# Optimization experiments

Measured on AMD Instinct MI355X. Metric: run time of the kernel, lower is better.

## Reference

```python
import jax, jax.numpy as jnp
import numpy as np

TEMP = 0.1
EPS = 1e-12  # F.normalize eps


def setup_inputs() -> dict:
    key = jax.random.key(0)
    k1, k2 = jax.random.split(key)
    B, C, N = 8, 128, 4096
    features = jax.random.normal(k1, (B, C, N), dtype=jnp.float32)
    labels_all = jax.random.randint(k2, (B, N), 0, 16, dtype=jnp.int32)
    return {"features": features, "labels_all": labels_all}


def _per_cloud_loss(features_map, labels):
    # features_map: [C, N], labels: [N]
    v = features_map.T  # [N, C]
    v = v / jnp.maximum(jnp.linalg.norm(v, axis=1, keepdims=True), EPS)
    dp = jnp.exp(jnp.matmul(v, v.T) / TEMP)  # [N, N]
    n = dp.shape[0]
    # remove diagonal (dot_products - diag(diagonal))
    dp = dp * (1.0 - jnp.eye(n, dtype=dp.dtype))
    mask = labels[:, None] == labels[None, :]  # [N, N]
    positives = jnp.sum(jnp.where(mask, dp, 0.0), axis=1)
    negatives = jnp.sum(jnp.where(mask, 0.0, dp), axis=1)
    deviation = -jnp.log(positives / (positives + negatives))
    return jnp.mean(deviation)


def reference(features, labels_all):
    # features: [B, C, N], labels_all: [B, N]
    losses = jax.vmap(_per_cloud_loss)(features, labels_all)  # [B]
    return jnp.mean(losses)
```

## Files before the change

kernel.cpp:

```cpp
#include <hip/hip_runtime.h>
#include <hip/hip_bf16.h>
#include <math.h>

#define BATCH 8
#define NPTS 4096
#define CH 128
#define CTG 4
#define CHUNK 32
#define NCHUNK (NPTS / (CTG * CHUNK))
#define NBUF 4

#define SQRT_TEMP_LOG2E 3.79828256f

typedef __attribute__((ext_vector_type(4))) float f32x4;
typedef __attribute__((ext_vector_type(4))) int   i32x4;
typedef __attribute__((ext_vector_type(8))) short bf16x8;

typedef __attribute__((address_space(3))) unsigned int lds_uint;
typedef __attribute__((address_space(1))) const unsigned int gbl_uint;

__device__ __forceinline__ void load_lds16(const void* g, const void* l) {
    __builtin_amdgcn_global_load_lds((gbl_uint*)g, (lds_uint*)l, 16, 0, 0);
}

__device__ __forceinline__ float fast_exp2(float x) {
    return __builtin_amdgcn_exp2f(x);
}

__global__ __launch_bounds__(256) void normalize_kernel(
    const float* __restrict__ f, __hip_bfloat16* __restrict__ vn,
    float* __restrict__ pos, float* __restrict__ neg, float* __restrict__ out)
{
    int idx = blockIdx.x * 256 + threadIdx.x;
    int point = idx >> 2, q = idx & 3;
    int b = point >> 12, n = point & (NPTS - 1);
    const float* base = f + (size_t)b * CH * NPTS + (size_t)(q * 32) * NPTS + n;

    float x[32];
    float ss = 0.0f;
    #pragma unroll
    for (int c = 0; c < 32; c++) {
        x[c] = base[(size_t)c * NPTS];
        ss += x[c] * x[c];
    }
    ss += __shfl_xor(ss, 1);
    ss += __shfl_xor(ss, 2);
    float scale = SQRT_TEMP_LOG2E / fmaxf(sqrtf(ss), 1e-12f);

    __hip_bfloat16* outp = vn + (size_t)point * CH + q * 32;
    #pragma unroll
    for (int c0 = 0; c0 < 32; c0 += 8) {
        union { __hip_bfloat16 h[8]; uint4 u; } pk;
        #pragma unroll
        for (int j = 0; j < 8; j++)
            pk.h[j] = __float2bfloat16(x[c0 + j] * scale);
        *((uint4*)(outp + c0)) = pk.u;
    }
    if (q == 0) pos[point] = 0.0f;
    else if (q == 1) neg[point] = 0.0f;
    if (idx == 0) out[0] = 0.0f;
}

__global__ __launch_bounds__(256, 4) void tile_kernel(
    const __hip_bfloat16* __restrict__ vn, const int* __restrict__ labels,
    float* __restrict__ pos, float* __restrict__ neg)
{
    __shared__ short lB[NBUF][CHUNK * CH];
    __shared__ int labL[NPTS / CTG];

    const int ctg = blockIdx.x, rt = blockIdx.y, b = blockIdx.z;
    const int tid = threadIdx.x;
    const int w = tid >> 6, lane = tid & 63;
    const int lane15 = lane & 15, quad = lane >> 4;

    const int row0 = rt * 128;
    const int colbase = ctg * (NPTS / CTG);
    const __hip_bfloat16* vb = vn + (size_t)b * NPTS * CH;
    const int* labb = labels + b * NPTS;

    auto STAGE = [&](int buf, int chunk) {
        const __hip_bfloat16* Bb = vb + (size_t)(colbase + chunk * CHUNK) * CH;
        #pragma unroll
        for (int i = 0; i < 2; i++) {
            int ldsrow = w * 8 + i * 4;
            int r = ldsrow + quad;
            int g = lane15 ^ (r & 15);
            load_lds16(Bb + (size_t)r * CH + g * 8, &lB[buf][ldsrow * CH]);
        }
    };

    load_lds16(labb + colbase + w * 256 + lane * 4, &labL[w * 256]);

    bf16x8 afrag[2][4];
    int lr[2];
    #pragma unroll
    for (int mi = 0; mi < 2; mi++) {
        const int row_l = w * 32 + mi * 16 + lane15;
        const __hip_bfloat16* Arow = vb + (size_t)(row0 + row_l) * CH;
        #pragma unroll
        for (int ks = 0; ks < 4; ks++)
            afrag[mi][ks] = *(const bf16x8*)(Arow + (ks * 4 + quad) * 8);
        lr[mi] = labb[row0 + row_l];
    }

    STAGE(0, 0);
    STAGE(1, 1);
    STAGE(2, 2);

    float pacc[2] = {0.0f, 0.0f}, tacc[2] = {0.0f, 0.0f};

    auto BODY = [&](int chunk, int buf) {
        STAGE((buf + 3) & (NBUF - 1), (chunk + 3) & (NCHUNK - 1));
        asm volatile("s_waitcnt vmcnt(6)" ::: "memory");
        __builtin_amdgcn_s_barrier();

        f32x4 acc[2][2] = {};
        __builtin_amdgcn_s_setprio(1);
        #pragma unroll
        for (int ks = 0; ks < 4; ks++) {
            const int koff = ((ks * 4 + quad) ^ lane15) << 3;
            #pragma unroll
            for (int ni = 0; ni < 2; ni++) {
                bf16x8 bf = *(const bf16x8*)&lB[buf][(ni * 16 + lane15) * CH + koff];
                acc[0][ni] = __builtin_amdgcn_mfma_f32_16x16x32_bf16(
                    bf, afrag[0][ks], acc[0][ni], 0, 0, 0);
                acc[1][ni] = __builtin_amdgcn_mfma_f32_16x16x32_bf16(
                    bf, afrag[1][ks], acc[1][ni], 0, 0, 0);
            }
        }
        __builtin_amdgcn_s_setprio(0);
        __builtin_amdgcn_s_barrier();

        #pragma unroll
        for (int ni = 0; ni < 2; ni++) {
            const i32x4 lc = *(const i32x4*)&labL[chunk * CHUNK + ni * 16 + quad * 4];
            const int colblk = colbase + chunk * CHUNK + ni * 16;
            #pragma unroll
            for (int mi = 0; mi < 2; mi++) {
                const bool dblk = (colblk == row0 + w * 32 + mi * 16);
                if (dblk) {
                    #pragma unroll
                    for (int r = 0; r < 4; r++) {
                        float e = fast_exp2(acc[mi][ni][r]);
                        if (lane15 == quad * 4 + r) e = 0.0f;
                        tacc[mi] += e;
                        pacc[mi] += (lc[r] == lr[mi]) ? e : 0.0f;
                    }
                } else {
                    #pragma unroll
                    for (int r = 0; r < 4; r++) {
                        float e = fast_exp2(acc[mi][ni][r]);
                        tacc[mi] += e;
                        pacc[mi] += (lc[r] == lr[mi]) ? e : 0.0f;
                    }
                }
            }
        }
    };

    #pragma unroll 1
    for (int c4 = 0; c4 < NCHUNK; c4 += 4) {
        BODY(c4 + 0, 0);
        BODY(c4 + 1, 1);
        BODY(c4 + 2, 2);
        BODY(c4 + 3, 3);
    }

    #pragma unroll
    for (int mi = 0; mi < 2; mi++) {
        float p = pacc[mi], tt = tacc[mi];
        p  += __shfl_xor(p, 16);   p  += __shfl_xor(p, 32);
        tt += __shfl_xor(tt, 16);  tt += __shfl_xor(tt, 32);
        if (lane < 16) {
            const int row_l = w * 32 + mi * 16 + lane15;
            atomicAdd(&pos[b * NPTS + row0 + row_l], p);
            atomicAdd(&neg[b * NPTS + row0 + row_l], tt - p);
        }
    }
}

__global__ __launch_bounds__(256) void finalize_kernel(
    const float* __restrict__ pos, const float* __restrict__ neg,
    float* __restrict__ out)
{
    int base = blockIdx.x * 1024 + threadIdx.x;
    float acc = 0.0f;
    #pragma unroll
    for (int k = 0; k < 4; k++) {
        int i = base + k * 256;
        float p = pos[i];
        float t = p + neg[i];
        acc += __logf(t / p);
    }
    #pragma unroll
    for (int off = 32; off; off >>= 1) acc += __shfl_down(acc, off);
    __shared__ float red[4];
    if ((threadIdx.x & 63) == 0) red[threadIdx.x >> 6] = acc;
    __syncthreads();
    if (threadIdx.x == 0) {
        float v = red[0] + red[1] + red[2] + red[3];
        atomicAdd(out, v * (1.0f / (BATCH * NPTS)));
    }
}

extern "C" void kernel_launch(void* const* d_in, const int* in_sizes, int n_in,
                              void* d_out, int out_size, void* d_ws, size_t ws_size,
                              hipStream_t stream)
{
    const float* features = (const float*)d_in[0];
    const int*   labels   = (const int*)d_in[1];
    float*       out      = (float*)d_out;

    __hip_bfloat16* vn = (__hip_bfloat16*)d_ws;
    float* pos = (float*)((char*)d_ws + (size_t)BATCH * NPTS * CH * sizeof(__hip_bfloat16));
    float* neg = pos + BATCH * NPTS;

    hipLaunchKernelGGL(normalize_kernel, dim3(BATCH * NPTS * 4 / 256), dim3(256), 0, stream,
                       features, vn, pos, neg, out);
    hipLaunchKernelGGL(tile_kernel, dim3(CTG, 32, BATCH), dim3(256), 0, stream,
                       vn, labels, pos, neg);
    hipLaunchKernelGGL(finalize_kernel, dim3(32), dim3(256), 0, stream, pos, neg, out);
}
```

Measured before the change: 112.8 us.

## Software-pipeline MFMA and exp epilogue across chunks; normalize two points per thread

```diff
diff --git a/kernel.cpp b/kernel.cpp
--- a/kernel.cpp
+++ b/kernel.cpp
@@ -32,32 +32,42 @@
     float* __restrict__ pos, float* __restrict__ neg, float* __restrict__ out)
 {
     int idx = blockIdx.x * 256 + threadIdx.x;
-    int point = idx >> 2, q = idx & 3;
-    int b = point >> 12, n = point & (NPTS - 1);
-    const float* base = f + (size_t)b * CH * NPTS + (size_t)(q * 32) * NPTS + n;
-
-    float x[32];
-    float ss = 0.0f;
+    int pp = idx >> 2, q = idx & 3;
+    int b = pp >> 11, n2 = (pp & 2047) * 2;
+    const float* base = f + (size_t)b * CH * NPTS + (size_t)(q * 32) * NPTS + n2;
+
+    float x0[32], x1[32];
+    float s0 = 0.0f, s1 = 0.0f;
     #pragma unroll
     for (int c = 0; c < 32; c++) {
-        x[c] = base[(size_t)c * NPTS];
-        ss += x[c] * x[c];
-    }
-    ss += __shfl_xor(ss, 1);
-    ss += __shfl_xor(ss, 2);
-    float scale = SQRT_TEMP_LOG2E / fmaxf(sqrtf(ss), 1e-12f);
-
-    __hip_bfloat16* outp = vn + (size_t)point * CH + q * 32;
+        float2 v = *(const float2*)(base + (size_t)c * NPTS);
+        x0[c] = v.x; x1[c] = v.y;
+        s0 += v.x * v.x; s1 += v.y * v.y;
+    }
+    s0 += __shfl_xor(s0, 1); s0 += __shfl_xor(s0, 2);
+    s1 += __shfl_xor(s1, 1); s1 += __shfl_xor(s1, 2);
+    float sc0 = SQRT_TEMP_LOG2E / fmaxf(sqrtf(s0), 1e-12f);
+    float sc1 = SQRT_TEMP_LOG2E / fmaxf(sqrtf(s1), 1e-12f);
+
+    int point = b * NPTS + n2;
+    __hip_bfloat16* o0 = vn + (size_t)point * CH + q * 32;
     #pragma unroll
     for (int c0 = 0; c0 < 32; c0 += 8) {
         union { __hip_bfloat16 h[8]; uint4 u; } pk;
         #pragma unroll
-        for (int j = 0; j < 8; j++)
-            pk.h[j] = __float2bfloat16(x[c0 + j] * scale);
-        *((uint4*)(outp + c0)) = pk.u;
-    }
-    if (q == 0) pos[point] = 0.0f;
-    else if (q == 1) neg[point] = 0.0f;
+        for (int j = 0; j < 8; j++) pk.h[j] = __float2bfloat16(x0[c0 + j] * sc0);
+        *((uint4*)(o0 + c0)) = pk.u;
+    }
+    __hip_bfloat16* o1 = o0 + CH;
+    #pragma unroll
+    for (int c0 = 0; c0 < 32; c0 += 8) {
+        union { __hip_bfloat16 h[8]; uint4 u; } pk;
+        #pragma unroll
+        for (int j = 0; j < 8; j++) pk.h[j] = __float2bfloat16(x1[c0 + j] * sc1);
+        *((uint4*)(o1 + c0)) = pk.u;
+    }
+    if (q == 0)      { pos[point] = 0.0f; pos[point + 1] = 0.0f; }
+    else if (q == 1) { neg[point] = 0.0f; neg[point + 1] = 0.0f; }
     if (idx == 0) out[0] = 0.0f;
 }
 
@@ -78,7 +88,7 @@
     const __hip_bfloat16* vb = vn + (size_t)b * NPTS * CH;
     const int* labb = labels + b * NPTS;
 
-    auto STAGE = [&](int buf, int chunk) {
+    auto stage = [&](int buf, int chunk) {
         const __hip_bfloat16* Bb = vb + (size_t)(colbase + chunk * CHUNK) * CH;
         #pragma unroll
         for (int i = 0; i < 2; i++) {
@@ -103,68 +113,109 @@
         lr[mi] = labb[row0 + row_l];
     }
 
-    STAGE(0, 0);
-    STAGE(1, 1);
-    STAGE(2, 2);
+    stage(0, 0);
+    stage(1, 1);
+    stage(2, 2);
+
+    int vad[2][4];
+    #pragma unroll
+    for (int ni = 0; ni < 2; ni++)
+        #pragma unroll
+        for (int ks = 0; ks < 4; ks++)
+            vad[ni][ks] = (((ni * 16 + lane15) * CH) +
+                           (((ks * 4 + quad) ^ lane15) << 3)) * 2;
 
     float pacc[2] = {0.0f, 0.0f}, tacc[2] = {0.0f, 0.0f};
-
-    auto BODY = [&](int chunk, int buf) {
-        STAGE((buf + 3) & (NBUF - 1), (chunk + 3) & (NCHUNK - 1));
-        asm volatile("s_waitcnt vmcnt(6)" ::: "memory");
-        __builtin_amdgcn_s_barrier();
-
-        f32x4 acc[2][2] = {};
-        __builtin_amdgcn_s_setprio(1);
-        #pragma unroll
-        for (int ks = 0; ks < 4; ks++) {
-            const int koff = ((ks * 4 + quad) ^ lane15) << 3;
-            #pragma unroll
-            for (int ni = 0; ni < 2; ni++) {
-                bf16x8 bf = *(const bf16x8*)&lB[buf][(ni * 16 + lane15) * CH + koff];
-                acc[0][ni] = __builtin_amdgcn_mfma_f32_16x16x32_bf16(
-                    bf, afrag[0][ks], acc[0][ni], 0, 0, 0);
-                acc[1][ni] = __builtin_amdgcn_mfma_f32_16x16x32_bf16(
-                    bf, afrag[1][ks], acc[1][ni], 0, 0, 0);
-            }
-        }
-        __builtin_amdgcn_s_setprio(0);
-        __builtin_amdgcn_s_barrier();
-
-        #pragma unroll
-        for (int ni = 0; ni < 2; ni++) {
-            const i32x4 lc = *(const i32x4*)&labL[chunk * CHUNK + ni * 16 + quad * 4];
-            const int colblk = colbase + chunk * CHUNK + ni * 16;
-            #pragma unroll
-            for (int mi = 0; mi < 2; mi++) {
-                const bool dblk = (colblk == row0 + w * 32 + mi * 16);
-                if (dblk) {
-                    #pragma unroll
-                    for (int r = 0; r < 4; r++) {
-                        float e = fast_exp2(acc[mi][ni][r]);
-                        if (lane15 == quad * 4 + r) e = 0.0f;
-                        tacc[mi] += e;
-                        pacc[mi] += (lc[r] == lr[mi]) ? e : 0.0f;
-                    }
-                } else {
-                    #pragma unroll
-                    for (int r = 0; r < 4; r++) {
-                        float e = fast_exp2(acc[mi][ni][r]);
-                        tacc[mi] += e;
-                        pacc[mi] += (lc[r] == lr[mi]) ? e : 0.0f;
-                    }
-                }
-            }
-        }
-    };
-
+    const f32x4 zf = {0.0f, 0.0f, 0.0f, 0.0f};
+    f32x4 accA[2][2], accB[2][2];
+
+#define MFMA_PH(BUF_, ACC_)                                                   \
+    {                                                                         \
+        _Pragma("unroll")                                                     \
+        for (int ni = 0; ni < 2; ni++) {                                      \
+            bf16x8 bf = *(const bf16x8*)((const char*)(&lB[0][0]) +           \
+                         (BUF_) * (CHUNK * CH * 2) + vad[ni][0]);             \
+            ACC_[0][ni] = __builtin_amdgcn_mfma_f32_16x16x32_bf16(            \
+                bf, afrag[0][0], zf, 0, 0, 0);                                \
+            ACC_[1][ni] = __builtin_amdgcn_mfma_f32_16x16x32_bf16(            \
+                bf, afrag[1][0], zf, 0, 0, 0);                                \
+        }                                                                     \
+        _Pragma("unroll")                                                     \
+        for (int ks = 1; ks < 4; ks++) {                                      \
+            _Pragma("unroll")                                                 \
+            for (int ni = 0; ni < 2; ni++) {                                  \
+                bf16x8 bf = *(const bf16x8*)((const char*)(&lB[0][0]) +       \
+                             (BUF_) * (CHUNK * CH * 2) + vad[ni][ks]);        \
+                ACC_[0][ni] = __builtin_amdgcn_mfma_f32_16x16x32_bf16(        \
+                    bf, afrag[0][ks], ACC_[0][ni], 0, 0, 0);                  \
+                ACC_[1][ni] = __builtin_amdgcn_mfma_f32_16x16x32_bf16(        \
+                    bf, afrag[1][ks], ACC_[1][ni], 0, 0, 0);                  \
+            }                                                                 \
+        }                                                                     \
+    }
+
+#define EPI_PH(EC_, ACC_)                                                     \
+    {                                                                         \
+        _Pragma("unroll")                                                     \
+        for (int ni = 0; ni < 2; ni++) {                                      \
+            const i32x4 lc = *(const i32x4*)&labL[(EC_) * CHUNK + ni * 16 +   \
+                                                  quad * 4];                  \
+            const int colblk = colbase + (EC_) * CHUNK + ni * 16;             \
+            _Pragma("unroll")                                                 \
+            for (int mi = 0; mi < 2; mi++) {                                  \
+                const bool dblk = (colblk == row0 + w * 32 + mi * 16);        \
+                if (dblk) {                                                   \
+                    _Pragma("unroll")                                         \
+                    for (int r = 0; r < 4; r++) {                             \
+                        float e = fast_exp2(ACC_[mi][ni][r]);                 \
+                        if (lane15 == quad * 4 + r) e = 0.0f;   \
+                        tacc[mi] += e;                                        \
+                        pacc[mi] += (lc[r] == lr[mi]) ? e : 0.0f;             \
+                    }                                                         \
+                } else {                                                      \
+                    _Pragma("unroll")                                         \
+                    for (int r = 0; r < 4; r++) {                             \
+                        float e = fast_exp2(ACC_[mi][ni][r]);                 \
+                        tacc[mi] += e;                                        \
+                        pacc[mi] += (lc[r] == lr[mi]) ? e : 0.0f;             \
+                    }                                                         \
+                }                                                             \
+            }                                                                 \
+        }                                                                     \
+    }
+
+#define BODY(C_, BUF_, CUR_, PRV_, DOEPI_)                                    \
+    {                                                                         \
+        __builtin_amdgcn_s_barrier();                                         \
+        __builtin_amdgcn_s_setprio(1);                                        \
+        MFMA_PH(BUF_, CUR_);                                                  \
+        stage(((BUF_) + 3) & 3, ((C_) + 3) & (NCHUNK - 1));                   \
+        if (DOEPI_) { EPI_PH((C_) - 1, PRV_); }                               \
+        __builtin_amdgcn_s_setprio(0);                                        \
+        asm volatile("s_waitcnt vmcnt(4)" ::: "memory");                      \
+    }
+
+    asm volatile("s_waitcnt vmcnt(4)" ::: "memory");
+    BODY(0, 0, accA, accB, 0);
     #pragma unroll 1
-    for (int c4 = 0; c4 < NCHUNK; c4 += 4) {
-        BODY(c4 + 0, 0);
-        BODY(c4 + 1, 1);
-        BODY(c4 + 2, 2);
-        BODY(c4 + 3, 3);
-    }
+    for (int c = 1; c < 29; c += 4) {
+        BODY(c + 0, 1, accB, accA, 1);
+        BODY(c + 1, 2, accA, accB, 1);
+        BODY(c + 2, 3, accB, accA, 1);
+        BODY(c + 3, 0, accA, accB, 1);
+    }
+    BODY(29, 1, accB, accA, 1);
+    BODY(30, 2, accA, accB, 1);
+    __builtin_amdgcn_s_barrier();
+    __builtin_amdgcn_s_setprio(1);
+    MFMA_PH(3, accB);
+    EPI_PH(30, accA);
+    __builtin_amdgcn_s_setprio(0);
+    EPI_PH(31, accB);
+
+#undef BODY
+#undef EPI_PH
+#undef MFMA_PH
 
     #pragma unroll
     for (int mi = 0; mi < 2; mi++) {
@@ -215,7 +266,7 @@
     float* pos = (float*)((char*)d_ws + (size_t)BATCH * NPTS * CH * sizeof(__hip_bfloat16));
     float* neg = pos + BATCH * NPTS;
 
-    hipLaunchKernelGGL(normalize_kernel, dim3(BATCH * NPTS * 4 / 256), dim3(256), 0, stream,
+    hipLaunchKernelGGL(normalize_kernel, dim3(BATCH * NPTS * 2 / 256), dim3(256), 0, stream,
                        features, vn, pos, neg, out);
     hipLaunchKernelGGL(tile_kernel, dim3(CTG, 32, BATCH), dim3(256), 0, stream,
                        vn, labels, pos, neg);
```

Result: slower. 116.0 us (+2.8%).
